# Kernel tuning notes

Hardware: AMD Instinct MI355X
Metric: run time of the kernel (lower is better)

The kernel has to match this reference:

```python
import jax, jax.numpy as jnp
import numpy as np


def setup_inputs() -> dict:
    key = jax.random.key(0)
    ks = jax.random.split(key, 6)
    C, C8, W, H, B = 512, 64, 64, 64, 4
    x = jax.random.normal(ks[0], (B, C, W, H), dtype=jnp.float32)
    Wf = jax.random.normal(ks[1], (C8, C), dtype=jnp.float32) * (1.0 / np.sqrt(C))
    Wg = jax.random.normal(ks[2], (C8, C), dtype=jnp.float32) * (1.0 / np.sqrt(C))
    Wh = jax.random.normal(ks[3], (C8, C), dtype=jnp.float32) * (1.0 / np.sqrt(C))
    Wv = jax.random.normal(ks[4], (C, C8), dtype=jnp.float32) * (1.0 / np.sqrt(C8))
    gamma = jax.random.normal(ks[5], (1,), dtype=jnp.float32)
    return {"x": x, "Wf": Wf, "Wg": Wg, "Wh": Wh, "Wv": Wv, "gamma": gamma}


def reference(x, Wf, Wg, Wh, Wv, gamma):
    b, c, w, h = x.shape
    n = w * h
    xf = x.reshape(b, c, n)                       # [b, c, n]
    # 1x1 convs == channel-mixing GEMMs
    f = jnp.einsum('oc,bcn->bon', Wf, xf)         # [b, c8, n]
    g = jnp.einsum('oc,bcn->bon', Wg, xf)         # [b, c8, n]
    hmap = jnp.einsum('oc,bcn->bon', Wh, xf)      # [b, c8, n]
    # attn_map[b, i, j] = sum_c f[b, c, i] * g[b, c, j]  (f permuted as in torch)
    attn = jnp.einsum('bci,bcj->bij', f, g)       # [b, n, n]
    # unconventional softmax over dim=1 (rows / the i axis)
    attn = jax.nn.softmax(attn, axis=1)
    sa = jnp.einsum('bcn,bnj->bcj', hmap, attn)   # [b, c8, n]
    sa = sa.reshape(b, -1, w, h)                  # [b, c8, w, h]
    sa = jnp.einsum('oc,bcwh->bowh', Wv, sa)      # [b, c, w, h]
    out = sa * gamma[0] + x
    return out, sa
```

## Files before the change

kernel.cpp:

```cpp
#include <hip/hip_runtime.h>
#include <cstddef>

#define BB 4
#define CC 512
#define NN 4096

using half8  = __attribute__((ext_vector_type(8))) _Float16;
using fp16x2 = __attribute__((ext_vector_type(2))) __fp16;
using short8 = __attribute__((ext_vector_type(8))) short;
using us8    = __attribute__((ext_vector_type(8))) unsigned short;
using f32x4  = __attribute__((ext_vector_type(4))) float;
using f32x16 = __attribute__((ext_vector_type(16))) float;

__device__ __forceinline__ unsigned short f2bf(float x) {
    unsigned int u = __float_as_uint(x);
    u += 0x7fffu + ((u >> 16) & 1u);
    return (unsigned short)(u >> 16);
}

__global__ __launch_bounds__(256) void prep_kernel(
    const float* __restrict__ Wf, const float* __restrict__ Wg,
    const float* __restrict__ Wh, const float* __restrict__ Wv,
    _Float16* __restrict__ Wc16, _Float16* __restrict__ Wv16)
{
    int idx = blockIdx.x * 256 + threadIdx.x;
    int stride = gridDim.x * 256;
    const int N1 = 192 * 512, N2 = 512 * 64;
    for (int i = idx; i < N1 + N2; i += stride) {
        if (i < N1) {
            int row = i >> 9, c = i & 511;
            const float* src = (row < 64) ? Wf : ((row < 128) ? Wg : Wh);
            float sc = (row >= 64 && row < 128) ? 1.4426950408889634f : 1.0f;
            Wc16[i] = (_Float16)(sc * src[(row & 63) * 512 + c]);
        } else {
            int k = i - N1;
            Wv16[k] = (_Float16)Wv[k];
        }
    }
}

__global__ __launch_bounds__(256) void proj_kernel(
    const float* __restrict__ x, const _Float16* __restrict__ Wc16,
    _Float16* __restrict__ Kf, _Float16* __restrict__ Qf,
    unsigned short* __restrict__ Vt)
{
    __shared__ float xsT[2][32][68];
    const int t    = threadIdx.x;
    const int w    = t >> 6;
    const int lane = t & 63;
    const int lh   = lane & 15;
    const int qd   = lane >> 4;
    const int b    = blockIdx.x >> 7;
    const int i0   = (blockIdx.x & 127) << 5;

    f32x4 acc[3][2];
    #pragma unroll
    for (int ot = 0; ot < 3; ot++)
        #pragma unroll
        for (int it = 0; it < 2; it++) { acc[ot][it][0]=0.f; acc[ot][it][1]=0.f; acc[ot][it][2]=0.f; acc[ot][it][3]=0.f; }

    const int ti8 = t & 7;
    const int tc2 = t >> 3;
    const float* xbase = x + (size_t)b*CC*NN + i0 + ti8*4;
    const _Float16* wbase = Wc16 + (size_t)(w*48 + lh)*512 + qd*8;

    float4 st0, st1;
    half8  wcur[2][3], wnxt[2][3];

#define LOADX(ck) do {                                                        \
    st0 = *(const float4*)(xbase + (size_t)((ck)*64 + tc2)*NN);               \
    st1 = *(const float4*)(xbase + (size_t)((ck)*64 + 32 + tc2)*NN);          \
} while (0)
#define STOREX(p_) do {                                                       \
    xsT[p_][ti8*4+0][tc2]    = st0.x; xsT[p_][ti8*4+1][tc2]    = st0.y;       \
    xsT[p_][ti8*4+2][tc2]    = st0.z; xsT[p_][ti8*4+3][tc2]    = st0.w;       \
    xsT[p_][ti8*4+0][32+tc2] = st1.x; xsT[p_][ti8*4+1][32+tc2] = st1.y;       \
    xsT[p_][ti8*4+2][32+tc2] = st1.z; xsT[p_][ti8*4+3][32+tc2] = st1.w;       \
} while (0)
#define LOADW(ck, WD) do {                                                    \
    _Pragma("unroll")                                                         \
    for (int ks_ = 0; ks_ < 2; ks_++)                                         \
        _Pragma("unroll")                                                     \
        for (int ot_ = 0; ot_ < 3; ot_++)                                     \
            WD[ks_][ot_] = *(const half8*)(wbase + (size_t)(ot_*16)*512 + (ck)*64 + ks_*32); \
} while (0)

    LOADX(0); STOREX(0);
    LOADW(0, wcur);
    __syncthreads();

    #pragma unroll
    for (int ck = 0; ck < 8; ck++) {
        const int p = ck & 1;
        if (ck < 7) { LOADX(ck + 1); LOADW(ck + 1, wnxt); }

        #pragma unroll
        for (int ks = 0; ks < 2; ks++) {
            half8 xf[2];
            #pragma unroll
            for (int it = 0; it < 2; it++) {
                const float* xr = &xsT[p][it*16 + lh][ks*32 + qd*8];
                f32x4 xa = *(const f32x4*)xr;
                f32x4 xb = *(const f32x4*)(xr + 4);
                union { fp16x2 h2[4]; half8 h8; } u;
                u.h2[0] = __builtin_amdgcn_cvt_pkrtz(xa[0], xa[1]);
                u.h2[1] = __builtin_amdgcn_cvt_pkrtz(xa[2], xa[3]);
                u.h2[2] = __builtin_amdgcn_cvt_pkrtz(xb[0], xb[1]);
                u.h2[3] = __builtin_amdgcn_cvt_pkrtz(xb[2], xb[3]);
                xf[it] = u.h8;
            }
            #pragma unroll
            for (int ot = 0; ot < 3; ot++)
                #pragma unroll
                for (int it = 0; it < 2; it++)
                    acc[ot][it] = __builtin_amdgcn_mfma_f32_16x16x32_f16(wcur[ks][ot], xf[it], acc[ot][it], 0, 0, 0);
        }

        if (ck < 7) {
            STOREX(p ^ 1);
            #pragma unroll
            for (int ks_ = 0; ks_ < 2; ks_++)
                #pragma unroll
                for (int ot_ = 0; ot_ < 3; ot_++)
                    wcur[ks_][ot_] = wnxt[ks_][ot_];
        }
        __syncthreads();
    }
#undef LOADX
#undef STOREX
#undef LOADW

    #pragma unroll
    for (int ot = 0; ot < 3; ot++) {
        int g16 = w*3 + ot;
        int m   = g16 >> 2;
        int obase = (g16 & 3)*16 + qd*4;
        #pragma unroll
        for (int it = 0; it < 2; it++) {
            int ig = i0 + it*16 + lh;
            #pragma unroll
            for (int r = 0; r < 4; r++) {
                float v = acc[ot][it][r];
                int ol = obase + r;
                if (m == 0)       Kf[((size_t)b*NN + ig)*64 + ol] = (_Float16)v;
                else if (m == 1)  Qf[((size_t)b*NN + ig)*64 + ol] = (_Float16)v;
                else              Vt[((size_t)b*64 + ol)*NN + ig] = f2bf(v);
            }
        }
    }
}

template<int SPLITS>
__global__ __launch_bounds__(256, 3) void attn_kernel(
    const _Float16* __restrict__ Kf, const _Float16* __restrict__ Qf,
    const unsigned short* __restrict__ Vt,
    _Float16* __restrict__ Po16, float* __restrict__ Pl)
{
    static_assert(NN % SPLITS == 0, "split");
    constexpr int KS  = NN / SPLITS;
    constexpr int NCH = KS / 64;
    static_assert(NCH >= 3, "need >=3 chunks for 3-buffer pipeline");

    __shared__ __align__(16) unsigned short Kb2[3][64*64];
    __shared__ __align__(16) unsigned short Vb2[3][64*64];

    const int t    = threadIdx.x;
    const int wv   = t >> 6;
    const int lane = t & 63;
    const int il   = lane & 31;
    const int h    = lane >> 5;

    const int p  = blockIdx.x;
    const int v  = (p & 7) * (SPLITS * 16) + (p >> 3);
    const int jt = v & 31;
    const int bs = v >> 5;
    const int b  = bs / SPLITS;
    const int s  = bs % SPLITS;
    const int j0w  = jt*128 + wv*32;
    const int koff = s * KS;

    half8 qfr[4];
    {
        const _Float16* qp = Qf + ((size_t)b*NN + j0w + il)*64 + h*8;
        #pragma unroll
        for (int sl = 0; sl < 4; sl++) qfr[sl] = *(const half8*)(qp + sl*16);
    }

    f32x16 o_acc[2];
    #pragma unroll
    for (int dt = 0; dt < 2; dt++)
        #pragma unroll
        for (int r = 0; r < 16; r++) o_acc[dt][r] = 0.f;
    float l4[4] = {0.f, 0.f, 0.f, 0.f};

    const int slot0 = t, slot1 = 256 + t;
    const int ik0 = slot0 >> 3, sw0 = ((slot0 & 7) ^ (ik0 & 7)) << 3;
    const int ik1 = slot1 >> 3, sw1 = ((slot1 & 7) ^ (ik1 & 7)) << 3;
    const _Float16*       gk0 = Kf + ((size_t)b*NN + koff + ik0)*64 + sw0;
    const _Float16*       gk1 = Kf + ((size_t)b*NN + koff + ik1)*64 + sw1;
    const unsigned short* gv0 = Vt + ((size_t)b*64 + ik0)*NN + koff + sw0;
    const unsigned short* gv1 = Vt + ((size_t)b*64 + ik1)*NN + koff + sw1;

#define STAGE(ck, pb) do {                                                          \
    const size_t o64_ = (size_t)(ck)*64;                                            \
    __builtin_amdgcn_global_load_lds(                                               \
        (const __attribute__((address_space(1))) void*)(gk0 + o64_*64),             \
        (__attribute__((address_space(3))) void*)&Kb2[pb][(wv*64)*8], 16, 0, 0);    \
    __builtin_amdgcn_global_load_lds(                                               \
        (const __attribute__((address_space(1))) void*)(gk1 + o64_*64),             \
        (__attribute__((address_space(3))) void*)&Kb2[pb][(256 + wv*64)*8], 16, 0, 0); \
    __builtin_amdgcn_global_load_lds(                                               \
        (const __attribute__((address_space(1))) void*)(gv0 + o64_),                \
        (__attribute__((address_space(3))) void*)&Vb2[pb][(wv*64)*8], 16, 0, 0);    \
    __builtin_amdgcn_global_load_lds(                                               \
        (const __attribute__((address_space(1))) void*)(gv1 + o64_),                \
        (__attribute__((address_space(3))) void*)&Vb2[pb][(256 + wv*64)*8], 16, 0, 0); \
    } while (0)

    STAGE(0, 0);
    STAGE(1, 1);
    asm volatile("s_waitcnt vmcnt(4)" ::: "memory");
    __builtin_amdgcn_sched_barrier(0);
    __builtin_amdgcn_s_barrier();
    __builtin_amdgcn_sched_barrier(0);

    int cb = 0, nb = 2;
    for (int ck = 0; ck < NCH; ck++) {
        if (ck + 2 < NCH) STAGE(ck + 2, nb);

        const unsigned short* Kb = Kb2[cb];
        const unsigned short* Vb = Vb2[cb];

        #pragma unroll
        for (int isub = 0; isub < 2; isub++) {
            const int irow = isub*32 + il;
            const unsigned short* kr = Kb + irow*64;
            f32x16 sc;
            #pragma unroll
            for (int r = 0; r < 16; r++) sc[r] = 0.f;
            __builtin_amdgcn_s_setprio(1);
            #pragma unroll
            for (int sl = 0; sl < 4; sl++) {
                half8 kf = *(const half8*)(kr + (((sl*2 + h) ^ (irow & 7)) << 3));
                sc = __builtin_amdgcn_mfma_f32_32x32x16_f16(kf, qfr[sl], sc, 0, 0, 0);
            }
            __builtin_amdgcn_s_setprio(0);

            #pragma unroll
            for (int r = 0; r < 16; r++) sc[r] = exp2f(sc[r]);
            #pragma unroll
            for (int r = 0; r < 16; r++) l4[r & 3] += sc[r];

            unsigned wA[8];
            #pragma unroll
            for (int k = 0; k < 8; k++)
                asm("v_cvt_pk_bf16_f32 %0, %1, %2" : "=v"(wA[k]) : "v"(sc[2*k]), "v"(sc[2*k+1]));
            asm("v_permlane32_swap_b32 %0, %1" : "+v"(wA[0]), "+v"(wA[2]));
            asm("v_permlane32_swap_b32 %0, %1" : "+v"(wA[1]), "+v"(wA[3]));
            asm("v_permlane32_swap_b32 %0, %1" : "+v"(wA[4]), "+v"(wA[6]));
            asm("v_permlane32_swap_b32 %0, %1" : "+v"(wA[5]), "+v"(wA[7]));

            union { unsigned u[4]; short8 s8; } pa0, pa1;
            pa0.u[0]=wA[0]; pa0.u[1]=wA[1]; pa0.u[2]=wA[2]; pa0.u[3]=wA[3];
            pa1.u[0]=wA[4]; pa1.u[1]=wA[5]; pa1.u[2]=wA[6]; pa1.u[3]=wA[7];

            __builtin_amdgcn_s_setprio(1);
            #pragma unroll
            for (int isl = 0; isl < 2; isl++) {
                const short8 paf = isl ? pa1.s8 : pa0.s8;
                const int vc = isub*4 + isl*2 + h;
                #pragma unroll
                for (int dt = 0; dt < 2; dt++) {
                    const int drow = dt*32 + il;
                    short8 vf = *(const short8*)(Vb + drow*64 + ((vc ^ (drow & 7)) << 3));
                    o_acc[dt] = __builtin_amdgcn_mfma_f32_32x32x16_bf16(paf, vf, o_acc[dt], 0, 0, 0);
                }
            }
            __builtin_amdgcn_s_setprio(0);
        }

        if (ck + 1 < NCH) {
            if (ck + 2 < NCH) asm volatile("s_waitcnt vmcnt(4)" ::: "memory");
            else              asm volatile("s_waitcnt vmcnt(0)" ::: "memory");
            __builtin_amdgcn_sched_barrier(0);
            __builtin_amdgcn_s_barrier();
            __builtin_amdgcn_sched_barrier(0);
        }

        cb = (cb == 2) ? 0 : cb + 1;
        nb = (nb == 2) ? 0 : nb + 1;
    }
#undef STAGE

    float l_acc  = (l4[0] + l4[1]) + (l4[2] + l4[3]);
    float l_full = l_acc + __shfl_xor(l_acc, 32);
    float inv = 1.0f / l_full;

    const size_t pbase = (size_t)(s*4 + b)*NN + j0w;
    #pragma unroll
    for (int r = 0; r < 16; r++) {
        const int jr = (r & 3) + 8*(r >> 2) + 4*h;
        const float invr = __shfl(inv, jr);
        #pragma unroll
        for (int dt = 0; dt < 2; dt++)
            Po16[(pbase + jr)*64 + dt*32 + il] = (_Float16)(o_acc[dt][r] * invr);
    }
    if (h == 0) Pl[pbase + il] = l_full;
}

template<int SPLITS>
__global__ __launch_bounds__(256) void outproj_kernel(
    const _Float16* __restrict__ Po16, const float* __restrict__ Pl,
    const _Float16* __restrict__ Wv16,
    const float* __restrict__ x, const float* __restrict__ gamma,
    float* __restrict__ out1, float* __restrict__ out2)
{
    __shared__ float Osh[4][16][20];
    const int t    = threadIdx.x;
    const int w    = t >> 6;
    const int lane = t & 63;
    const int lh   = lane & 15;
    const int qd   = lane >> 4;
    const int b    = blockIdx.x >> 8;
    const int j0   = (blockIdx.x & 255) << 4;
    const float g  = gamma[0];

    half8 sb0, sb1;
    {
        const int j = j0 + lh;
        float os[16];
        #pragma unroll
        for (int k = 0; k < 16; k++) os[k] = 0.f;
        float lsum = 0.f;
        #pragma unroll
        for (int s = 0; s < SPLITS; s++) {
            size_t base = ((size_t)(s*4 + b)*NN + j);
            half8 v0 = *(const half8*)(Po16 + base*64 + qd*8);
            half8 v1 = *(const half8*)(Po16 + base*64 + qd*8 + 32);
            float l = Pl[base];
            #pragma unroll
            for (int k = 0; k < 8; k++) {
                os[k]   = fmaf(l, (float)v0[k], os[k]);
                os[8+k] = fmaf(l, (float)v1[k], os[8+k]);
            }
            lsum += l;
        }
        float inv = 1.0f / lsum;
        union { fp16x2 h2[4]; half8 h8; } u0, u1;
        #pragma unroll
        for (int k = 0; k < 4; k++) {
            u0.h2[k] = __builtin_amdgcn_cvt_pkrtz(os[2*k]*inv,   os[2*k+1]*inv);
            u1.h2[k] = __builtin_amdgcn_cvt_pkrtz(os[8+2*k]*inv, os[8+2*k+1]*inv);
        }
        sb0 = u0.h8;
        sb1 = u1.h8;
    }

    const int o_loc = lane >> 2;
    const int j4    = (lane & 3) * 4;

    #pragma unroll 2
    for (int ot8 = 0; ot8 < 8; ot8++) {
        const int ot = w*8 + ot8;
        const size_t wbase = (size_t)(ot*16 + lh)*64 + qd*8;
        half8 a0 = *(const half8*)(Wv16 + wbase);
        half8 a1 = *(const half8*)(Wv16 + wbase + 32);

        f32x4 acc;
        acc[0]=0.f; acc[1]=0.f; acc[2]=0.f; acc[3]=0.f;
        acc = __builtin_amdgcn_mfma_f32_16x16x32_f16(a0, sb0, acc, 0, 0, 0);
        acc = __builtin_amdgcn_mfma_f32_16x16x32_f16(a1, sb1, acc, 0, 0, 0);

        #pragma unroll
        for (int r = 0; r < 4; r++)
            Osh[w][qd*4 + r][lh] = acc[r];
        asm volatile("s_waitcnt lgkmcnt(0)" ::: "memory");

        f32x4 vv = *(const f32x4*)&Osh[w][o_loc][j4];
        const int o  = ot*16 + o_loc;
        const size_t idx = ((size_t)b*CC + o)*NN + j0 + j4;
        f32x4 xv = *(const f32x4*)(x + idx);
        *(f32x4*)(out2 + idx) = vv;
        f32x4 r1;
        r1[0] = fmaf(g, vv[0], xv[0]); r1[1] = fmaf(g, vv[1], xv[1]);
        r1[2] = fmaf(g, vv[2], xv[2]); r1[3] = fmaf(g, vv[3], xv[3]);
        *(f32x4*)(out1 + idx) = r1;
        asm volatile("s_waitcnt lgkmcnt(0)" ::: "memory");
    }
}

extern "C" void kernel_launch(void* const* d_in, const int* in_sizes, int n_in,
                              void* d_out, int out_size, void* d_ws, size_t ws_size,
                              hipStream_t stream) {
    const float* x     = (const float*)d_in[0];
    const float* Wf    = (const float*)d_in[1];
    const float* Wg    = (const float*)d_in[2];
    const float* Wh    = (const float*)d_in[3];
    const float* Wv    = (const float*)d_in[4];
    const float* gamma = (const float*)d_in[5];

    float* out1 = (float*)d_out;
    float* out2 = out1 + (size_t)BB*CC*NN;

    const size_t BND = (size_t)BB*NN*64;
    const size_t need8 = BND*2*3 + BND*2*8 + (size_t)8*BB*NN*4
                       + (size_t)192*512*2 + (size_t)512*64*2;
    const int SPL = (ws_size >= need8) ? 8 : 4;

    char* wp = (char*)d_ws;
    _Float16*       Kf   = (_Float16*)wp;        wp += BND*2;
    _Float16*       Qf   = (_Float16*)wp;        wp += BND*2;
    unsigned short* Vt   = (unsigned short*)wp;  wp += BND*2;
    _Float16*       Po16 = (_Float16*)wp;        wp += BND*2*SPL;
    float*          Pl   = (float*)wp;           wp += (size_t)SPL*BB*NN*4;
    _Float16*       Wc16 = (_Float16*)wp;        wp += (size_t)192*512*2;
    _Float16*       Wv16 = (_Float16*)wp;

    prep_kernel<<<dim3(64), dim3(256), 0, stream>>>(Wf, Wg, Wh, Wv, Wc16, Wv16);
    proj_kernel<<<dim3(BB*128), dim3(256), 0, stream>>>(x, Wc16, Kf, Qf, Vt);
    if (SPL == 8) {
        attn_kernel<8><<<dim3(128*8), dim3(256), 0, stream>>>(Kf, Qf, Vt, Po16, Pl);
        outproj_kernel<8><<<dim3(BB*256), dim3(256), 0, stream>>>(Po16, Pl, Wv16, x, gamma, out1, out2);
    } else {
        attn_kernel<4><<<dim3(128*4), dim3(256), 0, stream>>>(Kf, Qf, Vt, Po16, Pl);
        outproj_kernel<4><<<dim3(BB*256), dim3(256), 0, stream>>>(Po16, Pl, Wv16, x, gamma, out1, out2);
    }
}
```

Baseline: 170.4 us.

## Use double-buffered LDS attention pipeline and dedupe split-merge in outproj

The attention kernel drops from a three-buffer LDS pipeline with manual vmcnt waits and s_setprio hints to a simpler two-buffer scheme with __syncthreads, and changes the LDS swizzle to a different XOR pattern. It also puts the exp results in a separate array instead of reusing the score register. The output-projection kernel now merges the split partials once per block into shared memory rather than redundantly across all four waves, and hoists the x load earlier to overlap with the MFMA work. The smaller LDS footprint may raise occupancy, but prefetch depth is reduced and the extra barrier per chunk may expose load latency.

```diff
diff --git a/kernel.cpp b/kernel.cpp
--- a/kernel.cpp
+++ b/kernel.cpp
@@ -159,10 +159,9 @@
     static_assert(NN % SPLITS == 0, "split");
     constexpr int KS  = NN / SPLITS;
     constexpr int NCH = KS / 64;
-    static_assert(NCH >= 3, "need >=3 chunks for 3-buffer pipeline");
-
-    __shared__ __align__(16) unsigned short Kb2[3][64*64];
-    __shared__ __align__(16) unsigned short Vb2[3][64*64];
+
+    __shared__ __align__(16) unsigned short Kb2[2][64*64];
+    __shared__ __align__(16) unsigned short Vb2[2][64*64];
 
     const int t    = threadIdx.x;
     const int wv   = t >> 6;
@@ -193,13 +192,16 @@
         for (int r = 0; r < 16; r++) o_acc[dt][r] = 0.f;
     float l4[4] = {0.f, 0.f, 0.f, 0.f};
 
-    const int slot0 = t, slot1 = 256 + t;
-    const int ik0 = slot0 >> 3, sw0 = ((slot0 & 7) ^ (ik0 & 7)) << 3;
-    const int ik1 = slot1 >> 3, sw1 = ((slot1 & 7) ^ (ik1 & 7)) << 3;
-    const _Float16*       gk0 = Kf + ((size_t)b*NN + koff + ik0)*64 + sw0;
-    const _Float16*       gk1 = Kf + ((size_t)b*NN + koff + ik1)*64 + sw1;
-    const unsigned short* gv0 = Vt + ((size_t)b*64 + ik0)*NN + koff + sw0;
-    const unsigned short* gv1 = Vt + ((size_t)b*64 + ik1)*NN + koff + sw1;
+    const int fx = (il & 7) ^ ((il >> 3) & 3);
+
+    const int ik0 = t >> 3;
+    const int fk0 = (ik0 & 7) ^ ((ik0 >> 3) & 3);
+    const int sw  = ((t & 7) ^ fk0) << 3;
+    const int ik1 = ik0 + 32;
+    const _Float16*       gk0 = Kf + ((size_t)b*NN + koff + ik0)*64 + sw;
+    const _Float16*       gk1 = Kf + ((size_t)b*NN + koff + ik1)*64 + sw;
+    const unsigned short* gv0 = Vt + ((size_t)b*64 + ik0)*NN + koff + sw;
+    const unsigned short* gv1 = Vt + ((size_t)b*64 + ik1)*NN + koff + sw;
 
 #define STAGE(ck, pb) do {                                                          \
     const size_t o64_ = (size_t)(ck)*64;                                            \
@@ -218,15 +220,11 @@
     } while (0)
 
     STAGE(0, 0);
-    STAGE(1, 1);
-    asm volatile("s_waitcnt vmcnt(4)" ::: "memory");
-    __builtin_amdgcn_sched_barrier(0);
-    __builtin_amdgcn_s_barrier();
-    __builtin_amdgcn_sched_barrier(0);
-
-    int cb = 0, nb = 2;
+    __syncthreads();
+
     for (int ck = 0; ck < NCH; ck++) {
-        if (ck + 2 < NCH) STAGE(ck + 2, nb);
+        const int cb = ck & 1;
+        if (ck + 1 < NCH) STAGE(ck + 1, cb ^ 1);
 
         const unsigned short* Kb = Kb2[cb];
         const unsigned short* Vb = Vb2[cb];
@@ -238,23 +236,22 @@
             f32x16 sc;
             #pragma unroll
             for (int r = 0; r < 16; r++) sc[r] = 0.f;
-            __builtin_amdgcn_s_setprio(1);
             #pragma unroll
             for (int sl = 0; sl < 4; sl++) {
-                half8 kf = *(const half8*)(kr + (((sl*2 + h) ^ (irow & 7)) << 3));
+                half8 kf = *(const half8*)(kr + (((sl*2 + h) ^ fx) << 3));
                 sc = __builtin_amdgcn_mfma_f32_32x32x16_f16(kf, qfr[sl], sc, 0, 0, 0);
             }
-            __builtin_amdgcn_s_setprio(0);
-
-            #pragma unroll
-            for (int r = 0; r < 16; r++) sc[r] = exp2f(sc[r]);
-            #pragma unroll
-            for (int r = 0; r < 16; r++) l4[r & 3] += sc[r];
+
+            float pq[16];
+            #pragma unroll
+            for (int r = 0; r < 16; r++) pq[r] = exp2f(sc[r]);
+            #pragma unroll
+            for (int r = 0; r < 16; r++) l4[r & 3] += pq[r];
 
             unsigned wA[8];
             #pragma unroll
             for (int k = 0; k < 8; k++)
-                asm("v_cvt_pk_bf16_f32 %0, %1, %2" : "=v"(wA[k]) : "v"(sc[2*k]), "v"(sc[2*k+1]));
+                asm("v_cvt_pk_bf16_f32 %0, %1, %2" : "=v"(wA[k]) : "v"(pq[2*k]), "v"(pq[2*k+1]));
             asm("v_permlane32_swap_b32 %0, %1" : "+v"(wA[0]), "+v"(wA[2]));
             asm("v_permlane32_swap_b32 %0, %1" : "+v"(wA[1]), "+v"(wA[3]));
             asm("v_permlane32_swap_b32 %0, %1" : "+v"(wA[4]), "+v"(wA[6]));
@@ -264,7 +261,6 @@
             pa0.u[0]=wA[0]; pa0.u[1]=wA[1]; pa0.u[2]=wA[2]; pa0.u[3]=wA[3];
             pa1.u[0]=wA[4]; pa1.u[1]=wA[5]; pa1.u[2]=wA[6]; pa1.u[3]=wA[7];
 
-            __builtin_amdgcn_s_setprio(1);
             #pragma unroll
             for (int isl = 0; isl < 2; isl++) {
                 const short8 paf = isl ? pa1.s8 : pa0.s8;
@@ -272,23 +268,12 @@
                 #pragma unroll
                 for (int dt = 0; dt < 2; dt++) {
                     const int drow = dt*32 + il;
-                    short8 vf = *(const short8*)(Vb + drow*64 + ((vc ^ (drow & 7)) << 3));
+                    short8 vf = *(const short8*)(Vb + drow*64 + ((vc ^ fx) << 3));
                     o_acc[dt] = __builtin_amdgcn_mfma_f32_32x32x16_bf16(paf, vf, o_acc[dt], 0, 0, 0);
                 }
             }
-            __builtin_amdgcn_s_setprio(0);
-        }
-
-        if (ck + 1 < NCH) {
-            if (ck + 2 < NCH) asm volatile("s_waitcnt vmcnt(4)" ::: "memory");
-            else              asm volatile("s_waitcnt vmcnt(0)" ::: "memory");
-            __builtin_amdgcn_sched_barrier(0);
-            __builtin_amdgcn_s_barrier();
-            __builtin_amdgcn_sched_barrier(0);
-        }
-
-        cb = (cb == 2) ? 0 : cb + 1;
-        nb = (nb == 2) ? 0 : nb + 1;
+        }
+        __syncthreads();
     }
 #undef STAGE
 
@@ -315,6 +300,7 @@
     const float* __restrict__ x, const float* __restrict__ gamma,
     float* __restrict__ out1, float* __restrict__ out2)
 {
+    __shared__ __align__(16) _Float16 sbM[16][72];
     __shared__ float Osh[4][16][20];
     const int t    = threadIdx.x;
     const int w    = t >> 6;
@@ -325,36 +311,32 @@
     const int j0   = (blockIdx.x & 255) << 4;
     const float g  = gamma[0];
 
-    half8 sb0, sb1;
-    {
-        const int j = j0 + lh;
-        float os[16];
-        #pragma unroll
-        for (int k = 0; k < 16; k++) os[k] = 0.f;
+    if (t < 128) {
+        const int jj = t & 15, d8 = t >> 4;
+        float os[8];
+        #pragma unroll
+        for (int k = 0; k < 8; k++) os[k] = 0.f;
         float lsum = 0.f;
         #pragma unroll
         for (int s = 0; s < SPLITS; s++) {
-            size_t base = ((size_t)(s*4 + b)*NN + j);
-            half8 v0 = *(const half8*)(Po16 + base*64 + qd*8);
-            half8 v1 = *(const half8*)(Po16 + base*64 + qd*8 + 32);
-            float l = Pl[base];
-            #pragma unroll
-            for (int k = 0; k < 8; k++) {
-                os[k]   = fmaf(l, (float)v0[k], os[k]);
-                os[8+k] = fmaf(l, (float)v1[k], os[8+k]);
-            }
+            const size_t base = (size_t)(s*4 + b)*NN + j0 + jj;
+            half8 vv = *(const half8*)(Po16 + base*64 + d8*8);
+            float l  = Pl[base];
+            #pragma unroll
+            for (int k = 0; k < 8; k++) os[k] = fmaf(l, (float)vv[k], os[k]);
             lsum += l;
         }
-        float inv = 1.0f / lsum;
-        union { fp16x2 h2[4]; half8 h8; } u0, u1;
-        #pragma unroll
-        for (int k = 0; k < 4; k++) {
-            u0.h2[k] = __builtin_amdgcn_cvt_pkrtz(os[2*k]*inv,   os[2*k+1]*inv);
-            u1.h2[k] = __builtin_amdgcn_cvt_pkrtz(os[8+2*k]*inv, os[8+2*k+1]*inv);
-        }
-        sb0 = u0.h8;
-        sb1 = u1.h8;
-    }
+        const float inv = 1.0f / lsum;
+        union { fp16x2 h2[4]; half8 h8; } u;
+        #pragma unroll
+        for (int k = 0; k < 4; k++)
+            u.h2[k] = __builtin_amdgcn_cvt_pkrtz(os[2*k]*inv, os[2*k+1]*inv);
+        *(half8*)&sbM[jj][d8*8] = u.h8;
+    }
+    __syncthreads();
+
+    const half8 sb0 = *(const half8*)&sbM[lh][qd*8];
+    const half8 sb1 = *(const half8*)&sbM[lh][32 + qd*8];
 
     const int o_loc = lane >> 2;
     const int j4    = (lane & 3) * 4;
@@ -362,6 +344,10 @@
     #pragma unroll 2
     for (int ot8 = 0; ot8 < 8; ot8++) {
         const int ot = w*8 + ot8;
+
+        const size_t idx = ((size_t)b*CC + ot*16 + o_loc)*NN + j0 + j4;
+        const f32x4 xv = *(const f32x4*)(x + idx);
+
         const size_t wbase = (size_t)(ot*16 + lh)*64 + qd*8;
         half8 a0 = *(const half8*)(Wv16 + wbase);
         half8 a1 = *(const half8*)(Wv16 + wbase + 32);
@@ -377,9 +363,6 @@
         asm volatile("s_waitcnt lgkmcnt(0)" ::: "memory");
 
         f32x4 vv = *(const f32x4*)&Osh[w][o_loc][j4];
-        const int o  = ot*16 + o_loc;
-        const size_t idx = ((size_t)b*CC + o)*NN + j0 + j4;
-        f32x4 xv = *(const f32x4*)(x + idx);
         *(f32x4*)(out2 + idx) = vv;
         f32x4 r1;
         r1[0] = fmaf(g, vv[0], xv[0]); r1[1] = fmaf(g, vv[1], xv[1]);
```

After: 164.6 us. 1.04x faster.
